# Optimization experiments

Measured on AMD Instinct MI355X. Metric: run time of the kernel, lower is better.

The kernel has to match this reference:

```python
import jax, jax.numpy as jnp
import numpy as np

D_MODEL = 32   # channels arg = Mamba d_model
D_INNER = 32   # expand=1
D_STATE = 8
DT_RANK = 2    # ceil(32/16)
D_CONV = 4


def layer_norm(h, g, b, eps=1e-5):
    m = jnp.mean(h, axis=-1, keepdims=True)
    v = jnp.var(h, axis=-1, keepdims=True)
    return (h - m) * jax.lax.rsqrt(v + eps) * g + b


def causal_conv1d(h, w, b):
    # h: [B, d, L]; w: [d, K] depthwise; torch Conv1d(padding=K-1) truncated to first L
    out = jax.lax.conv_general_dilated(h, w[:, None, :], (1,), [(D_CONV - 1, 0)],
                                       dimension_numbers=('NCH', 'OIH', 'NCH'),
                                       feature_group_count=h.shape[1])
    return out + b[None, :, None]


def selective_scan(u, delta, A, Bm, Cm, D):
    # u, delta: [B, d, L]; A: [d, n]; Bm, Cm: [B, n, L]; D: [d]
    dA = jnp.exp(jnp.einsum('bdl,dn->lbdn', delta, A))       # [L, B, d, n]
    dBu = jnp.einsum('bdl,bnl,bdl->lbdn', delta, Bm, u)      # [L, B, d, n]
    Cseq = jnp.transpose(Cm, (2, 0, 1))                      # [L, B, n]
    h0 = jnp.zeros((u.shape[0], A.shape[0], A.shape[1]), u.dtype)

    def step(h, inp):
        dA_t, dBu_t, C_t = inp
        h = dA_t * h + dBu_t
        return h, jnp.einsum('bdn,bn->bd', h, C_t)

    _, ys = jax.lax.scan(step, h0, (dA, dBu, Cseq))          # ys: [L, B, d]
    return jnp.transpose(ys, (1, 2, 0)) + D[None, :, None] * u


def mamba_direction(xz, conv_w, conv_b, xproj_w, dtproj_w, dtproj_b, A_log, D):
    xh, z = jnp.split(xz, 2, axis=1)                         # each [B, d_inner, L]
    xh = jax.nn.silu(causal_conv1d(xh, conv_w, conv_b))
    x_dbl = jnp.einsum('bdl,kd->bkl', xh, xproj_w)           # [B, dt_rank+2n, L]
    dt, Bm, Cm = jnp.split(x_dbl, [DT_RANK, DT_RANK + D_STATE], axis=1)
    dt = jax.nn.softplus(jnp.einsum('brl,dr->bdl', dt, dtproj_w) + dtproj_b[None, :, None])
    y = selective_scan(xh, dt, -jnp.exp(A_log), Bm, Cm, D)
    return y * jax.nn.silu(z)


def forward(x, lin1_w, lin1_b, ln1_g, ln1_b, in_proj_w,
            conv_w_f, conv_b_f, xproj_w_f, dtproj_w_f, dtproj_b_f, A_log_f, D_f,
            conv_w_r, conv_b_r, xproj_w_r, dtproj_w_r, dtproj_b_r, A_log_r, D_r,
            out_proj_w, mnorm_g, mnorm_b, lin2_w, lin2_b):
    avg = jnp.mean(x, axis=(2, 3))                           # [B, C] adaptive avg pool
    mx = jnp.max(x, axis=(2, 3))                             # [B, C] adaptive max pool
    combined = jnp.stack([avg, mx], axis=-1)                 # [B, C, 2]
    h = combined @ lin1_w.T + lin1_b                         # [B, C, d_model]
    h = layer_norm(h, ln1_g, ln1_b)
    # bidirectional Mamba (bimamba v2) over sequence length L = C
    xz = jnp.einsum('blc,ec->bel', h, in_proj_w)             # [B, 2*d_inner, L]
    out_f = mamba_direction(xz, conv_w_f, conv_b_f, xproj_w_f, dtproj_w_f, dtproj_b_f, A_log_f, D_f)
    out_r = mamba_direction(xz[..., ::-1], conv_w_r, conv_b_r, xproj_w_r, dtproj_w_r, dtproj_b_r, A_log_r, D_r)[..., ::-1]
    out = (out_f + out_r) / 2.0                              # if_devide_out=True
    out = jnp.einsum('bdl,od->blo', out, out_proj_w)         # [B, L, d_model]
    out = layer_norm(out, mnorm_g, mnorm_b)                  # use_norm=True
    att = jax.nn.sigmoid(out @ lin2_w.T + lin2_b)            # [B, L, 1]
    return att[..., None] * 0.25 + 0.875                     # [B, C, 1, 1]


def setup_inputs() -> dict:
    key = jax.random.key(0)
    ks = jax.random.split(key, 12)
    B, C, H, W = 32, 512, 64, 64

    def rn(k, shape, s):
        return jax.random.normal(k, shape, jnp.float32) * s

    A_log = jnp.log(jnp.broadcast_to(jnp.arange(1, D_STATE + 1, dtype=jnp.float32), (D_INNER, D_STATE)))
    return {
        'x': jax.random.normal(ks[0], (B, C, H, W), jnp.float32),
        'lin1_w': rn(ks[1], (D_MODEL, 2), 0.5),
        'lin1_b': jnp.zeros((D_MODEL,), jnp.float32),
        'ln1_g': jnp.ones((D_MODEL,), jnp.float32),
        'ln1_b': jnp.zeros((D_MODEL,), jnp.float32),
        'in_proj_w': rn(ks[2], (2 * D_INNER, D_MODEL), 0.1),
        'conv_w_f': rn(ks[3], (D_INNER, D_CONV), 0.3),
        'conv_b_f': jnp.zeros((D_INNER,), jnp.float32),
        'xproj_w_f': rn(ks[4], (DT_RANK + 2 * D_STATE, D_INNER), 0.1),
        'dtproj_w_f': rn(ks[5], (D_INNER, DT_RANK), 0.5),
        'dtproj_b_f': jnp.full((D_INNER,), -4.6, jnp.float32),
        'A_log_f': A_log,
        'D_f': jnp.ones((D_INNER,), jnp.float32),
        'conv_w_r': rn(ks[6], (D_INNER, D_CONV), 0.3),
        'conv_b_r': jnp.zeros((D_INNER,), jnp.float32),
        'xproj_w_r': rn(ks[7], (DT_RANK + 2 * D_STATE, D_INNER), 0.1),
        'dtproj_w_r': rn(ks[8], (D_INNER, DT_RANK), 0.5),
        'dtproj_b_r': jnp.full((D_INNER,), -4.6, jnp.float32),
        'A_log_r': A_log,
        'D_r': jnp.ones((D_INNER,), jnp.float32),
        'out_proj_w': rn(ks[9], (D_MODEL, D_INNER), 0.1),
        'mnorm_g': jnp.ones((D_MODEL,), jnp.float32),
        'mnorm_b': jnp.zeros((D_MODEL,), jnp.float32),
        'lin2_w': rn(ks[10], (1, D_MODEL), 0.3),
        'lin2_b': jnp.zeros((1,), jnp.float32),
    }


def reference(x, lin1_w, lin1_b, ln1_g, ln1_b, in_proj_w,
              conv_w_f, conv_b_f, xproj_w_f, dtproj_w_f, dtproj_b_f, A_log_f, D_f,
              conv_w_r, conv_b_r, xproj_w_r, dtproj_w_r, dtproj_b_r, A_log_r, D_r,
              out_proj_w, mnorm_g, mnorm_b, lin2_w, lin2_b):
    return forward(x, lin1_w, lin1_b, ln1_g, ln1_b, in_proj_w,
                   conv_w_f, conv_b_f, xproj_w_f, dtproj_w_f, dtproj_b_f, A_log_f, D_f,
                   conv_w_r, conv_b_r, xproj_w_r, dtproj_w_r, dtproj_b_r, A_log_r, D_r,
                   out_proj_w, mnorm_g, mnorm_b, lin2_w, lin2_b)
```

## Files before the change

kernel.cpp:

```cpp
#include <hip/hip_runtime.h>
#include <math.h>

#define BB 32
#define CC 512
#define HW 4096
#define DM 32
#define DI 32
#define DS 8
#define KC 4

__device__ __forceinline__ float siluf(float x) {
    return x / (1.0f + __expf(-x));
}
__device__ __forceinline__ float softplusf(float x) {
    float ax = fabsf(x);
    return fmaxf(x, 0.0f) + log1pf(__expf(-ax));
}

__global__ __launch_bounds__(256) void pool_kernel(const float* __restrict__ x,
                                                   float* __restrict__ avg,
                                                   float* __restrict__ mx) {
    int bc = blockIdx.x;
    const float4* xp = reinterpret_cast<const float4*>(x + (size_t)bc * HW);
    int tid = threadIdx.x;
    float s = 0.f, m = -INFINITY;
#pragma unroll
    for (int r = 0; r < 4; ++r) {
        float4 v = xp[r * 256 + tid];
        s += (v.x + v.y) + (v.z + v.w);
        m = fmaxf(m, fmaxf(fmaxf(v.x, v.y), fmaxf(v.z, v.w)));
    }
    for (int off = 32; off > 0; off >>= 1) {
        s += __shfl_down(s, off);
        m = fmaxf(m, __shfl_down(m, off));
    }
    __shared__ float ss[4], sm[4];
    int wave = tid >> 6;
    if ((tid & 63) == 0) { ss[wave] = s; sm[wave] = m; }
    __syncthreads();
    if (tid == 0) {
        float S = (ss[0] + ss[1]) + (ss[2] + ss[3]);
        float M = fmaxf(fmaxf(sm[0], sm[1]), fmaxf(sm[2], sm[3]));
        avg[bc] = S * (1.0f / HW);
        mx[bc]  = M;
    }
}

__global__ __launch_bounds__(256) void hproj_kernel(
    const float* __restrict__ avg, const float* __restrict__ mx,
    const float* __restrict__ lin1_w, const float* __restrict__ lin1_b,
    const float* __restrict__ ln1_g, const float* __restrict__ ln1_b,
    const float* __restrict__ in_proj_w, float* __restrict__ xz)
{
    int bx = blockIdx.x;
    int lb = bx >> 2, eg = bx & 3;
    __shared__ float sW[16 * DM];
    int tid = threadIdx.x;
    for (int i = tid; i < 16 * DM; i += 256) sW[i] = in_proj_w[eg * 16 * DM + i];
    __syncthreads();
    int g = lb * 256 + tid;
    int b = g >> 9, l = g & 511;
    float a = avg[g], M = mx[g];
    float h[DM];
    float mean = 0.f;
#pragma unroll
    for (int m_ = 0; m_ < DM; ++m_) {
        h[m_] = a * lin1_w[2 * m_] + M * lin1_w[2 * m_ + 1] + lin1_b[m_];
        mean += h[m_];
    }
    mean *= (1.0f / DM);
    float var = 0.f;
#pragma unroll
    for (int m_ = 0; m_ < DM; ++m_) { float d = h[m_] - mean; var += d * d; }
    var *= (1.0f / DM);
    float rs = rsqrtf(var + 1e-5f);
#pragma unroll
    for (int m_ = 0; m_ < DM; ++m_)
        h[m_] = (h[m_] - mean) * rs * ln1_g[m_] + ln1_b[m_];
#pragma unroll
    for (int e2 = 0; e2 < 16; ++e2) {
        int e = eg * 16 + e2;
        float acc = 0.f;
#pragma unroll
        for (int m_ = 0; m_ < DM; ++m_) acc += h[m_] * sW[e2 * DM + m_];
        xz[(((size_t)b * 64 + e) << 9) + l] = acc;
    }
}

#define NCH2 8
#define CHL2 64
__global__ __launch_bounds__(256) void convscan1_kernel(
    const float* __restrict__ xz,
    const float* __restrict__ conv_w_f, const float* __restrict__ conv_b_f,
    const float* __restrict__ xproj_w_f, const float* __restrict__ dtproj_w_f,
    const float* __restrict__ dtproj_b_f,
    const float* __restrict__ conv_w_r, const float* __restrict__ conv_b_r,
    const float* __restrict__ xproj_w_r, const float* __restrict__ dtproj_w_r,
    const float* __restrict__ dtproj_b_r,
    const float* __restrict__ A_log_f, const float* __restrict__ A_log_r,
    float* __restrict__ u_g, float* __restrict__ dt_g,
    float* __restrict__ B_g, float* __restrict__ C_g,
    float* __restrict__ carrA, float* __restrict__ carrH)
{
    int bx = blockIdx.x;
    int bd = bx >> 3, j = bx & 7;
    int b = bd >> 1, dir = bd & 1;
    int tid = threadIdx.x;
    const float* cw = dir ? conv_w_r : conv_w_f;
    const float* cb = dir ? conv_b_r : conv_b_f;
    const float* xw = dir ? xproj_w_r : xproj_w_f;
    const float* dw = dir ? dtproj_w_r : dtproj_w_f;
    const float* db = dir ? dtproj_b_r : dtproj_b_f;
    const float* Alog = dir ? A_log_r : A_log_f;
    const float* xzb = xz + (size_t)b * 64 * 512;

    __shared__ float xt[32][69];
    __shared__ float xw_s[18][33];
    __shared__ float u_s[64][33];
    __shared__ float dt_s[64][33];
    __shared__ float B_s[64][9];
    __shared__ float C_s[64][9];
    __shared__ float dtr_s[64][2];

    for (int idx = tid; idx < 32 * 67; idx += 256) {
        int dd = idx / 67, t = idx - dd * 67;
        int sidx = j * CHL2 - 3 + t;
        float v = 0.f;
        if (sidx >= 0) {
            int orig = dir ? (511 - sidx) : sidx;
            v = xzb[(dd << 9) + orig];
        }
        xt[dd][t] = v;
    }
    for (int idx = tid; idx < 18 * 32; idx += 256)
        xw_s[idx >> 5][idx & 31] = xw[idx];
    __syncthreads();

    int l = tid >> 2, gq = tid & 3;
#pragma unroll
    for (int i = 0; i < 8; ++i) {
        int dd = gq * 8 + i;
        float acc = cb[dd];
#pragma unroll
        for (int k = 0; k < KC; ++k) acc += cw[dd * KC + k] * xt[dd][l + k];
        u_s[l][dd] = siluf(acc);
    }
    __syncthreads();

    size_t row8 = ((size_t)bd * 512 + j * CHL2 + l) * 8;
    for (int o = gq; o < 18; o += 4) {
        float acc = 0.f;
#pragma unroll
        for (int m_ = 0; m_ < 32; ++m_) acc += u_s[l][m_] * xw_s[o][m_];
        if (o < 2) dtr_s[l][o] = acc;
        else if (o < 10) { B_s[l][o - 2] = acc; B_g[row8 + (o - 2)] = acc; }
        else             { C_s[l][o - 10] = acc; C_g[row8 + (o - 10)] = acc; }
    }
    __syncthreads();

    size_t rowbase = ((size_t)bd * 512 + j * CHL2) * 32;
    for (int idx = tid; idx < CHL2 * 32; idx += 256) {
        int ll = idx >> 5, dd = idx & 31;
        float v = dtr_s[ll][0] * dw[dd * 2] + dtr_s[ll][1] * dw[dd * 2 + 1] + db[dd];
        float sp = softplusf(v);
        dt_s[ll][dd] = sp;
        dt_g[rowbase + idx] = sp;
        u_g[rowbase + idx] = u_s[ll][dd];
    }
    __syncthreads();

    int dd = tid >> 3, nn = tid & 7;
    float Aa = -__expf(Alog[tid]);
    float ap = 1.f, h = 0.f;
#pragma unroll 4
    for (int sl = 0; sl < CHL2; ++sl) {
        float dtv = dt_s[sl][dd];
        float uu  = u_s[sl][dd];
        float bm  = B_s[sl][nn];
        float dA  = __expf(dtv * Aa);
        ap *= dA;
        h = dA * h + dtv * uu * bm;
    }
    carrA[(size_t)bx * 256 + tid] = ap;
    carrH[(size_t)bx * 256 + tid] = h;
}

__global__ __launch_bounds__(128) void scan2final_kernel(
    const float* __restrict__ u_g, const float* __restrict__ dt_g,
    const float* __restrict__ B_g, const float* __restrict__ C_g,
    const float* __restrict__ carrA, const float* __restrict__ carrH,
    const float* __restrict__ A_log_f, const float* __restrict__ D_f,
    const float* __restrict__ A_log_r, const float* __restrict__ D_r,
    const float* __restrict__ xz,
    const float* __restrict__ out_proj_w, const float* __restrict__ mnorm_g,
    const float* __restrict__ mnorm_b, const float* __restrict__ lin2_w,
    const float* __restrict__ lin2_b, float* __restrict__ out)
{
    int bx = blockIdx.x;
    int b = bx >> 3, jt = bx & 7;
    int tid = threadIdx.x;
    int dir = tid >> 6;
    int r = tid & 63;
    int dd = r >> 1, nh = r & 1, n0 = nh * 4;
    int bd = b * 2 + dir;
    int jc = dir ? (7 - jt) : jt;

    const float* Alog = dir ? A_log_r : A_log_f;
    const float* Dp   = dir ? D_r : D_f;

    float A0 = -__expf(Alog[dd * 8 + n0 + 0]);
    float A1 = -__expf(Alog[dd * 8 + n0 + 1]);
    float A2 = -__expf(Alog[dd * 8 + n0 + 2]);
    float A3 = -__expf(Alog[dd * 8 + n0 + 3]);
    float Dd = Dp[dd];

    float h0 = 0.f, h1 = 0.f, h2 = 0.f, h3 = 0.f;
    for (int jj = 0; jj < jc; ++jj) {
        size_t cbase = ((size_t)(bd * 8 + jj)) * 256 + dd * 8 + n0;
        float4 av = *reinterpret_cast<const float4*>(carrA + cbase);
        float4 hv = *reinterpret_cast<const float4*>(carrH + cbase);
        h0 = av.x * h0 + hv.x;
        h1 = av.y * h1 + hv.y;
        h2 = av.z * h2 + hv.z;
        h3 = av.w * h3 + hv.w;
    }

    __shared__ float y_s[2][2][64][33];

    size_t sb = (size_t)bd * 512 + jc * CHL2;
#pragma unroll 4
    for (int sl = 0; sl < CHL2; ++sl) {
        size_t s32 = (sb + sl) * 32 + dd;
        float dtv = dt_g[s32];
        float uu  = u_g[s32];
        float4 Bv = *reinterpret_cast<const float4*>(B_g + (sb + sl) * 8 + n0);
        float4 Cv = *reinterpret_cast<const float4*>(C_g + (sb + sl) * 8 + n0);
        float dtu = dtv * uu;
        h0 = __expf(dtv * A0) * h0 + dtu * Bv.x;
        h1 = __expf(dtv * A1) * h1 + dtu * Bv.y;
        h2 = __expf(dtv * A2) * h2 + dtu * Bv.z;
        h3 = __expf(dtv * A3) * h3 + dtu * Bv.w;
        float py = h0 * Cv.x + h1 * Cv.y + h2 * Cv.z + h3 * Cv.w;
        if (nh == 0) py += Dd * uu;
        int ll = dir ? (63 - sl) : sl;
        y_s[dir][nh][ll][dd] = py;
    }
    __syncthreads();

    if (tid < 64) {
        int lo = jt * 64 + tid;
        float comb[DI];
#pragma unroll
        for (int d2 = 0; d2 < DI; ++d2) {
            float ys = y_s[0][0][tid][d2] + y_s[0][1][tid][d2]
                     + y_s[1][0][tid][d2] + y_s[1][1][tid][d2];
            float z = xz[(((size_t)(b * 64 + 32 + d2)) << 9) + lo];
            comb[d2] = 0.5f * ys * siluf(z);
        }
        float o[DM];
        float mean = 0.f;
#pragma unroll
        for (int oo = 0; oo < DM; ++oo) {
            float acc = 0.f;
#pragma unroll
            for (int d2 = 0; d2 < DI; ++d2) acc += comb[d2] * out_proj_w[oo * DI + d2];
            o[oo] = acc;
            mean += acc;
        }
        mean *= (1.0f / DM);
        float var = 0.f;
#pragma unroll
        for (int oo = 0; oo < DM; ++oo) { float df = o[oo] - mean; var += df * df; }
        var *= (1.0f / DM);
        float rs = rsqrtf(var + 1e-5f);
        float s = lin2_b[0];
#pragma unroll
        for (int oo = 0; oo < DM; ++oo) {
            float v = (o[oo] - mean) * rs * mnorm_g[oo] + mnorm_b[oo];
            s += v * lin2_w[oo];
        }
        float att = 1.0f / (1.0f + __expf(-s));
        out[(size_t)b * 512 + lo] = 0.25f * att + 0.875f;
    }
}

extern "C" void kernel_launch(void* const* d_in, const int* in_sizes, int n_in,
                              void* d_out, int out_size, void* d_ws, size_t ws_size,
                              hipStream_t stream)
{
    const float* x         = (const float*)d_in[0];
    const float* lin1_w    = (const float*)d_in[1];
    const float* lin1_b    = (const float*)d_in[2];
    const float* ln1_g     = (const float*)d_in[3];
    const float* ln1_b     = (const float*)d_in[4];
    const float* in_proj_w = (const float*)d_in[5];
    const float* conv_w_f  = (const float*)d_in[6];
    const float* conv_b_f  = (const float*)d_in[7];
    const float* xproj_w_f = (const float*)d_in[8];
    const float* dtproj_w_f= (const float*)d_in[9];
    const float* dtproj_b_f= (const float*)d_in[10];
    const float* A_log_f   = (const float*)d_in[11];
    const float* D_f       = (const float*)d_in[12];
    const float* conv_w_r  = (const float*)d_in[13];
    const float* conv_b_r  = (const float*)d_in[14];
    const float* xproj_w_r = (const float*)d_in[15];
    const float* dtproj_w_r= (const float*)d_in[16];
    const float* dtproj_b_r= (const float*)d_in[17];
    const float* A_log_r   = (const float*)d_in[18];
    const float* D_r       = (const float*)d_in[19];
    const float* out_proj_w= (const float*)d_in[20];
    const float* mnorm_g   = (const float*)d_in[21];
    const float* mnorm_b   = (const float*)d_in[22];
    const float* lin2_w    = (const float*)d_in[23];
    const float* lin2_b    = (const float*)d_in[24];

    float* ws   = (float*)d_ws;
    float* avg  = ws;
    float* mx   = ws + 16384;
    float* xz   = ws + 32768;
    float* u_g  = xz + 1048576;
    float* dt_g = u_g + 1048576;
    float* B_g  = dt_g + 1048576;
    float* C_g  = B_g + 262144;
    float* carrA= C_g + 262144;
    float* carrH= carrA + 131072;
    (void)ws_size; (void)in_sizes; (void)n_in; (void)out_size;

    pool_kernel<<<BB * CC, 256, 0, stream>>>(x, avg, mx);
    hproj_kernel<<<64 * 4, 256, 0, stream>>>(avg, mx, lin1_w, lin1_b, ln1_g, ln1_b, in_proj_w, xz);
    convscan1_kernel<<<BB * 2 * NCH2, 256, 0, stream>>>(
        xz, conv_w_f, conv_b_f, xproj_w_f, dtproj_w_f, dtproj_b_f,
        conv_w_r, conv_b_r, xproj_w_r, dtproj_w_r, dtproj_b_r,
        A_log_f, A_log_r, u_g, dt_g, B_g, C_g, carrA, carrH);
    scan2final_kernel<<<BB * NCH2, 128, 0, stream>>>(
        u_g, dt_g, B_g, C_g, carrA, carrH,
        A_log_f, D_f, A_log_r, D_r, xz,
        out_proj_w, mnorm_g, mnorm_b, lin2_w, lin2_b, (float*)d_out);
}
```

Before: 91.14 us.

## Fuse pooling with input projection and halve scan chunk length

Merges the pool kernel and the layernorm/in_proj kernel into one kernel. Each block reduces one (b,c) row, then computes lin1, layernorm with wave shuffles, and the 64 in_proj outputs. This removes a launch and the avg/max round trip through memory. The cost is that every block now loads the full in_proj weight into shared memory. The scan is also split into 16 chunks of 32 instead of 8 chunks of 64, doubling the blocks in the conv/scan and final kernels for more parallelism, at the cost of a longer carry-propagation loop.

```diff
diff --git a/kernel.cpp b/kernel.cpp
--- a/kernel.cpp
+++ b/kernel.cpp
@@ -9,6 +9,9 @@
 #define DS 8
 #define KC 4
 
+#define NCH 16
+#define CHL 32
+
 __device__ __forceinline__ float siluf(float x) {
     return x / (1.0f + __expf(-x));
 }
@@ -17,12 +20,21 @@
     return fmaxf(x, 0.0f) + log1pf(__expf(-ax));
 }
 
-__global__ __launch_bounds__(256) void pool_kernel(const float* __restrict__ x,
-                                                   float* __restrict__ avg,
-                                                   float* __restrict__ mx) {
+__global__ __launch_bounds__(256) void poolproj_kernel(
+    const float* __restrict__ x,
+    const float* __restrict__ lin1_w, const float* __restrict__ lin1_b,
+    const float* __restrict__ ln1_g, const float* __restrict__ ln1_b,
+    const float* __restrict__ in_proj_w, float* __restrict__ xz)
+{
     int bc = blockIdx.x;
+    int b = bc >> 9, l = bc & 511;
     const float4* xp = reinterpret_cast<const float4*>(x + (size_t)bc * HW);
     int tid = threadIdx.x;
+
+    __shared__ float sWp[64][33];
+    __shared__ float ss[4], sm[4];
+    __shared__ float h_s[DM];
+
     float s = 0.f, m = -INFINITY;
 #pragma unroll
     for (int r = 0; r < 4; ++r) {
@@ -30,65 +42,44 @@
         s += (v.x + v.y) + (v.z + v.w);
         m = fmaxf(m, fmaxf(fmaxf(v.x, v.y), fmaxf(v.z, v.w)));
     }
+    for (int i = tid; i < 64 * DM; i += 256) sWp[i >> 5][i & 31] = in_proj_w[i];
+
     for (int off = 32; off > 0; off >>= 1) {
         s += __shfl_down(s, off);
         m = fmaxf(m, __shfl_down(m, off));
     }
-    __shared__ float ss[4], sm[4];
     int wave = tid >> 6;
     if ((tid & 63) == 0) { ss[wave] = s; sm[wave] = m; }
     __syncthreads();
-    if (tid == 0) {
+
+    if (tid < 32) {
         float S = (ss[0] + ss[1]) + (ss[2] + ss[3]);
         float M = fmaxf(fmaxf(sm[0], sm[1]), fmaxf(sm[2], sm[3]));
-        avg[bc] = S * (1.0f / HW);
-        mx[bc]  = M;
-    }
-}
-
-__global__ __launch_bounds__(256) void hproj_kernel(
-    const float* __restrict__ avg, const float* __restrict__ mx,
-    const float* __restrict__ lin1_w, const float* __restrict__ lin1_b,
-    const float* __restrict__ ln1_g, const float* __restrict__ ln1_b,
-    const float* __restrict__ in_proj_w, float* __restrict__ xz)
-{
-    int bx = blockIdx.x;
-    int lb = bx >> 2, eg = bx & 3;
-    __shared__ float sW[16 * DM];
-    int tid = threadIdx.x;
-    for (int i = tid; i < 16 * DM; i += 256) sW[i] = in_proj_w[eg * 16 * DM + i];
-    __syncthreads();
-    int g = lb * 256 + tid;
-    int b = g >> 9, l = g & 511;
-    float a = avg[g], M = mx[g];
-    float h[DM];
-    float mean = 0.f;
-#pragma unroll
-    for (int m_ = 0; m_ < DM; ++m_) {
-        h[m_] = a * lin1_w[2 * m_] + M * lin1_w[2 * m_ + 1] + lin1_b[m_];
-        mean += h[m_];
-    }
-    mean *= (1.0f / DM);
-    float var = 0.f;
-#pragma unroll
-    for (int m_ = 0; m_ < DM; ++m_) { float d = h[m_] - mean; var += d * d; }
-    var *= (1.0f / DM);
-    float rs = rsqrtf(var + 1e-5f);
-#pragma unroll
-    for (int m_ = 0; m_ < DM; ++m_)
-        h[m_] = (h[m_] - mean) * rs * ln1_g[m_] + ln1_b[m_];
-#pragma unroll
-    for (int e2 = 0; e2 < 16; ++e2) {
-        int e = eg * 16 + e2;
+        float a = S * (1.0f / HW);
+        int m_ = tid;
+        float h = a * lin1_w[2 * m_] + M * lin1_w[2 * m_ + 1] + lin1_b[m_];
+        float sum = h;
+#pragma unroll
+        for (int mask = 1; mask < 32; mask <<= 1) sum += __shfl_xor(sum, mask);
+        float mean = sum * (1.0f / DM);
+        float d = h - mean;
+        float vs = d * d;
+#pragma unroll
+        for (int mask = 1; mask < 32; mask <<= 1) vs += __shfl_xor(vs, mask);
+        float rs = rsqrtf(vs * (1.0f / DM) + 1e-5f);
+        h_s[m_] = d * rs * ln1_g[m_] + ln1_b[m_];
+    }
+    __syncthreads();
+
+    if (tid < 64) {
+        int e = tid;
         float acc = 0.f;
 #pragma unroll
-        for (int m_ = 0; m_ < DM; ++m_) acc += h[m_] * sW[e2 * DM + m_];
+        for (int m_ = 0; m_ < DM; ++m_) acc += h_s[m_] * sWp[e][m_];
         xz[(((size_t)b * 64 + e) << 9) + l] = acc;
     }
 }
 
-#define NCH2 8
-#define CHL2 64
 __global__ __launch_bounds__(256) void convscan1_kernel(
     const float* __restrict__ xz,
     const float* __restrict__ conv_w_f, const float* __restrict__ conv_b_f,
@@ -103,7 +94,7 @@
     float* __restrict__ carrA, float* __restrict__ carrH)
 {
     int bx = blockIdx.x;
-    int bd = bx >> 3, j = bx & 7;
+    int bd = bx >> 4, j = bx & 15;
     int b = bd >> 1, dir = bd & 1;
     int tid = threadIdx.x;
     const float* cw = dir ? conv_w_r : conv_w_f;
@@ -114,17 +105,17 @@
     const float* Alog = dir ? A_log_r : A_log_f;
     const float* xzb = xz + (size_t)b * 64 * 512;
 
-    __shared__ float xt[32][69];
+    __shared__ float xt[32][39];
     __shared__ float xw_s[18][33];
-    __shared__ float u_s[64][33];
-    __shared__ float dt_s[64][33];
-    __shared__ float B_s[64][9];
-    __shared__ float C_s[64][9];
-    __shared__ float dtr_s[64][2];
-
-    for (int idx = tid; idx < 32 * 67; idx += 256) {
-        int dd = idx / 67, t = idx - dd * 67;
-        int sidx = j * CHL2 - 3 + t;
+    __shared__ float u_s[CHL][33];
+    __shared__ float dt_s[CHL][33];
+    __shared__ float B_s[CHL][9];
+    __shared__ float C_s[CHL][9];
+    __shared__ float dtr_s[CHL][2];
+
+    for (int idx = tid; idx < 32 * 35; idx += 256) {
+        int dd = idx / 35, t = idx - dd * 35;
+        int sidx = j * CHL - 3 + t;
         float v = 0.f;
         if (sidx >= 0) {
             int orig = dir ? (511 - sidx) : sidx;
@@ -136,10 +127,10 @@
         xw_s[idx >> 5][idx & 31] = xw[idx];
     __syncthreads();
 
-    int l = tid >> 2, gq = tid & 3;
-#pragma unroll
-    for (int i = 0; i < 8; ++i) {
-        int dd = gq * 8 + i;
+    int l = tid >> 3, g8 = tid & 7;
+#pragma unroll
+    for (int i = 0; i < 4; ++i) {
+        int dd = g8 * 4 + i;
         float acc = cb[dd];
 #pragma unroll
         for (int k = 0; k < KC; ++k) acc += cw[dd * KC + k] * xt[dd][l + k];
@@ -147,19 +138,18 @@
     }
     __syncthreads();
 
-    size_t row8 = ((size_t)bd * 512 + j * CHL2 + l) * 8;
-    for (int o = gq; o < 18; o += 4) {
+    for (int o = g8; o < 18; o += 8) {
         float acc = 0.f;
 #pragma unroll
         for (int m_ = 0; m_ < 32; ++m_) acc += u_s[l][m_] * xw_s[o][m_];
         if (o < 2) dtr_s[l][o] = acc;
-        else if (o < 10) { B_s[l][o - 2] = acc; B_g[row8 + (o - 2)] = acc; }
-        else             { C_s[l][o - 10] = acc; C_g[row8 + (o - 10)] = acc; }
-    }
-    __syncthreads();
-
-    size_t rowbase = ((size_t)bd * 512 + j * CHL2) * 32;
-    for (int idx = tid; idx < CHL2 * 32; idx += 256) {
+        else if (o < 10) B_s[l][o - 2] = acc;
+        else             C_s[l][o - 10] = acc;
+    }
+    __syncthreads();
+
+    size_t rowbase = ((size_t)bd * 512 + j * CHL) * 32;
+    for (int idx = tid; idx < CHL * 32; idx += 256) {
         int ll = idx >> 5, dd = idx & 31;
         float v = dtr_s[ll][0] * dw[dd * 2] + dtr_s[ll][1] * dw[dd * 2 + 1] + db[dd];
         float sp = softplusf(v);
@@ -167,13 +157,18 @@
         dt_g[rowbase + idx] = sp;
         u_g[rowbase + idx] = u_s[ll][dd];
     }
+    size_t base8 = ((size_t)bd * 512 + j * CHL) * 8;
+    if (tid < CHL * 8) {
+        B_g[base8 + tid] = B_s[tid >> 3][tid & 7];
+        C_g[base8 + tid] = C_s[tid >> 3][tid & 7];
+    }
     __syncthreads();
 
     int dd = tid >> 3, nn = tid & 7;
     float Aa = -__expf(Alog[tid]);
     float ap = 1.f, h = 0.f;
 #pragma unroll 4
-    for (int sl = 0; sl < CHL2; ++sl) {
+    for (int sl = 0; sl < CHL; ++sl) {
         float dtv = dt_s[sl][dd];
         float uu  = u_s[sl][dd];
         float bm  = B_s[sl][nn];
@@ -181,8 +176,8 @@
         ap *= dA;
         h = dA * h + dtv * uu * bm;
     }
-    carrA[(size_t)bx * 256 + tid] = ap;
-    carrH[(size_t)bx * 256 + tid] = h;
+    carrA[((size_t)bx << 8) + tid] = ap;
+    carrH[((size_t)bx << 8) + tid] = h;
 }
 
 __global__ __launch_bounds__(128) void scan2final_kernel(
@@ -197,13 +192,13 @@
     const float* __restrict__ lin2_b, float* __restrict__ out)
 {
     int bx = blockIdx.x;
-    int b = bx >> 3, jt = bx & 7;
+    int b = bx >> 4, t = bx & 15;
     int tid = threadIdx.x;
     int dir = tid >> 6;
     int r = tid & 63;
     int dd = r >> 1, nh = r & 1, n0 = nh * 4;
     int bd = b * 2 + dir;
-    int jc = dir ? (7 - jt) : jt;
+    int tt = dir ? (15 - t) : t;
 
     const float* Alog = dir ? A_log_r : A_log_f;
     const float* Dp   = dir ? D_r : D_f;
@@ -215,8 +210,8 @@
     float Dd = Dp[dd];
 
     float h0 = 0.f, h1 = 0.f, h2 = 0.f, h3 = 0.f;
-    for (int jj = 0; jj < jc; ++jj) {
-        size_t cbase = ((size_t)(bd * 8 + jj)) * 256 + dd * 8 + n0;
+    for (int jj = 0; jj < tt; ++jj) {
+        size_t cbase = (((size_t)bd * NCH + jj) << 8) + dd * 8 + n0;
         float4 av = *reinterpret_cast<const float4*>(carrA + cbase);
         float4 hv = *reinterpret_cast<const float4*>(carrH + cbase);
         h0 = av.x * h0 + hv.x;
@@ -225,11 +220,11 @@
         h3 = av.w * h3 + hv.w;
     }
 
-    __shared__ float y_s[2][2][64][33];
-
-    size_t sb = (size_t)bd * 512 + jc * CHL2;
+    __shared__ float y_s[2][2][CHL][33];
+
+    size_t sb = (size_t)bd * 512 + tt * CHL;
 #pragma unroll 4
-    for (int sl = 0; sl < CHL2; ++sl) {
+    for (int sl = 0; sl < CHL; ++sl) {
         size_t s32 = (sb + sl) * 32 + dd;
         float dtv = dt_g[s32];
         float uu  = u_g[s32];
@@ -242,13 +237,13 @@
         h3 = __expf(dtv * A3) * h3 + dtu * Bv.w;
         float py = h0 * Cv.x + h1 * Cv.y + h2 * Cv.z + h3 * Cv.w;
         if (nh == 0) py += Dd * uu;
-        int ll = dir ? (63 - sl) : sl;
+        int ll = dir ? (CHL - 1 - sl) : sl;
         y_s[dir][nh][ll][dd] = py;
     }
     __syncthreads();
 
-    if (tid < 64) {
-        int lo = jt * 64 + tid;
+    if (tid < CHL) {
+        int lo = t * CHL + tid;
         float comb[DI];
 #pragma unroll
         for (int d2 = 0; d2 < DI; ++d2) {
@@ -315,24 +310,21 @@
     const float* lin2_b    = (const float*)d_in[24];
 
     float* ws   = (float*)d_ws;
-    float* avg  = ws;
-    float* mx   = ws + 16384;
-    float* xz   = ws + 32768;
+    float* xz   = ws;
     float* u_g  = xz + 1048576;
     float* dt_g = u_g + 1048576;
     float* B_g  = dt_g + 1048576;
     float* C_g  = B_g + 262144;
     float* carrA= C_g + 262144;
-    float* carrH= carrA + 131072;
+    float* carrH= carrA + 262144;
     (void)ws_size; (void)in_sizes; (void)n_in; (void)out_size;
 
-    pool_kernel<<<BB * CC, 256, 0, stream>>>(x, avg, mx);
-    hproj_kernel<<<64 * 4, 256, 0, stream>>>(avg, mx, lin1_w, lin1_b, ln1_g, ln1_b, in_proj_w, xz);
-    convscan1_kernel<<<BB * 2 * NCH2, 256, 0, stream>>>(
+    poolproj_kernel<<<BB * CC, 256, 0, stream>>>(x, lin1_w, lin1_b, ln1_g, ln1_b, in_proj_w, xz);
+    convscan1_kernel<<<BB * 2 * NCH, 256, 0, stream>>>(
         xz, conv_w_f, conv_b_f, xproj_w_f, dtproj_w_f, dtproj_b_f,
         conv_w_r, conv_b_r, xproj_w_r, dtproj_w_r, dtproj_b_r,
         A_log_f, A_log_r, u_g, dt_g, B_g, C_g, carrA, carrH);
-    scan2final_kernel<<<BB * NCH2, 128, 0, stream>>>(
+    scan2final_kernel<<<BB * NCH, 128, 0, stream>>>(
         u_g, dt_g, B_g, C_g, carrA, carrH,
         A_log_f, D_f, A_log_r, D_r, xz,
         out_proj_w, mnorm_g, mnorm_b, lin2_w, lin2_b, (float*)d_out);
```

Result: slower. 93.21 us (+2.3%).
